# Performance work log

Hardware: AMD Instinct MI355X
Metric: run time of the kernel (lower is better)

Reference implementation:

```python
import jax, jax.numpy as jnp
import numpy as np

N_NODES = 50000   # number of graph nodes
N_EDGES = 800000  # avg degree 16
D_IN = 128
D_OUT = 128


def setup_inputs() -> dict:
    key = jax.random.key(0)
    k = jax.random.split(key, 5)
    seq = jax.random.normal(k[0], (N_NODES, D_IN), dtype=jnp.float32)
    # Linear weight, torch layout [out_dim, in_dim], xavier-ish scale
    W = jax.random.normal(k[1], (D_OUT, D_IN), dtype=jnp.float32) * (1.414 / np.sqrt(D_IN))
    b = jnp.zeros((D_OUT,), dtype=jnp.float32)  # bias init fill_(0.0)
    # COO sparse adjacency: out[row] += val * seq_proj[col]
    edge_row = jax.random.randint(k[2], (N_EDGES,), 0, N_NODES, dtype=jnp.int32)
    edge_col = jax.random.randint(k[3], (N_EDGES,), 0, N_NODES, dtype=jnp.int32)
    edge_val = jax.random.uniform(k[4], (N_EDGES,), dtype=jnp.float32)
    return {"seq": seq, "W": W, "b": b,
            "edge_row": edge_row, "edge_col": edge_col, "edge_val": edge_val}


def reference(seq, W, b, edge_row, edge_col, edge_val):
    # seq = self.fc(seq): [N, D_in] @ [D_in, D_out]
    h = seq @ W.T                                   # [N, D_out]
    # out = torch.spmm(adj, h): COO gather-scale-scatter
    msgs = h[edge_col] * edge_val[:, None]          # [E, D_out]
    out = jax.ops.segment_sum(msgs, edge_row, num_segments=N_NODES)  # [N, D_out]
    # bias add + relu (fused epilogue)
    return jax.nn.relu(out + b)
```

## Files before the change

### kernel.cpp

```cpp
#include <hip/hip_runtime.h>

#define NN 50000
#define NE 800000
#define DD 128

#define BK_SHIFT 8
#define NBUCK 196
#define CHUNK 2048
#define NCHUNK 391
#define NGB 782
#define ECAP 8192

#define OFF_H      0
#define OFF_EBIN   3200000
#define OFF_EPACK  6411264
#define OFF_END    9622528
#define OFF_CUR    9672528
#define WS_FULL_FLOATS 9672724

typedef short short8 __attribute__((ext_vector_type(8)));
typedef float f32x4 __attribute__((ext_vector_type(4)));
typedef unsigned int uint32x2 __attribute__((ext_vector_type(2)));

static __device__ __forceinline__ unsigned int f2bf(float x) {
    unsigned int u = __float_as_uint(x);
    return (u + 0x7fffu + ((u >> 16) & 1u)) >> 16;
}

__global__ __launch_bounds__(256) void k1_gemm_scatter(
        const float* __restrict__ seq, const float* __restrict__ W,
        unsigned short* __restrict__ h,
        const int* __restrict__ erow, const int* __restrict__ ecol,
        const float* __restrict__ eval,
        int* __restrict__ gcur, uint2* __restrict__ ebin) {
    __shared__ uint4 lds4[3072];
    char* lds = (char*)lds4;
    const int t = threadIdx.x;

    if (blockIdx.x < NCHUNK) {
        int* lh = (int*)lds4;
        const int chunk = blockIdx.x;
        for (int i = t; i < NBUCK; i += 256) lh[i] = 0;
        __syncthreads();
        const int e0 = chunk * CHUNK;
        for (int i = t; i < CHUNK; i += 256) {
            int e = e0 + i;
            if (e < NE) atomicAdd(&lh[erow[e] >> BK_SHIFT], 1);
        }
        __syncthreads();
        for (int i = t; i < NBUCK; i += 256) {
            int c = lh[i];
            lh[i] = c ? atomicAdd(&gcur[i], c) : 0;
        }
        __syncthreads();
        for (int i = t; i < CHUNK; i += 256) {
            int e = e0 + i;
            if (e < NE) {
                int r = erow[e], c = ecol[e];
                unsigned int vb = __float_as_uint(eval[e]);
                int k = r >> BK_SHIFT;
                int pos = atomicAdd(&lh[k], 1);
                if (pos < ECAP)
                    ebin[(size_t)k * ECAP + pos] =
                        make_uint2(((unsigned)r << 16) | (unsigned)c, vb);
            }
        }
        return;
    }

    const int base = (blockIdx.x - NCHUNK) * 64;
#define BS_OFF 16384

    {
        const int o = t >> 1, ksb = (t & 1) * 64;
        const float4* Wr = (const float4*)(W + o * 128 + ksb);
#pragma unroll
        for (int i = 0; i < 16; i += 2) {
            float4 x = Wr[i], y = Wr[i + 1];
            uint4 p;
            p.x = f2bf(x.x) | (f2bf(x.y) << 16);
            p.y = f2bf(x.z) | (f2bf(x.w) << 16);
            p.z = f2bf(y.x) | (f2bf(y.y) << 16);
            p.w = f2bf(y.z) | (f2bf(y.w) << 16);
            int byte = o * 256 + (ksb + i * 4) * 2;
            *(uint4*)(lds + BS_OFF + (byte ^ ((o & 7) << 4))) = p;
        }
    }
    {
        const int row = t >> 2, n = base + row;
        const int c0 = (t & 3) * 4;
        const float4* Sr = (const float4*)(seq + (size_t)n * 128);
        const bool ok = (n < NN);
#pragma unroll
        for (int i = 0; i < 4; ++i) {
            int cc = c0 + i;
            float4 x = ok ? Sr[cc * 2]     : make_float4(0.f, 0.f, 0.f, 0.f);
            float4 y = ok ? Sr[cc * 2 + 1] : make_float4(0.f, 0.f, 0.f, 0.f);
            uint4 p;
            p.x = f2bf(x.x) | (f2bf(x.y) << 16);
            p.y = f2bf(x.z) | (f2bf(x.w) << 16);
            p.z = f2bf(y.x) | (f2bf(y.y) << 16);
            p.w = f2bf(y.z) | (f2bf(y.w) << 16);
            int byte = row * 256 + cc * 16;
            *(uint4*)(lds + (byte ^ ((row & 7) << 4))) = p;
        }
    }
    __syncthreads();

    const int l = t & 63, wv = t >> 6;
    const int lr = l & 15, kg = l >> 4;
    const int arow = wv * 16 + lr;
    f32x4 acc[8] = {};

#pragma unroll
    for (int ks = 0; ks < 4; ++ks) {
        const int kbyte = ks * 64 + kg * 16;
        short8 av = *(short8*)(lds + ((arow * 256 + kbyte) ^ ((arow & 7) << 4)));
#pragma unroll
        for (int c = 0; c < 8; ++c) {
            const int o = c * 16 + lr;
            short8 bv = *(short8*)(lds + BS_OFF +
                                   ((o * 256 + kbyte) ^ ((o & 7) << 4)));
            acc[c] = __builtin_amdgcn_mfma_f32_16x16x32_bf16(av, bv, acc[c], 0, 0, 0);
        }
    }

#pragma unroll
    for (int c = 0; c < 8; ++c) {
#pragma unroll
        for (int r = 0; r < 4; ++r) {
            int n = base + wv * 16 + kg * 4 + r;
            if (n < NN)
                h[(size_t)n * DD + c * 16 + lr] = (unsigned short)f2bf(acc[c][r]);
        }
    }
}

__global__ __launch_bounds__(256) void csr_fill(const uint2* __restrict__ ebin,
                                                const int* __restrict__ gcur,
                                                int* __restrict__ endv,
                                                uint2* __restrict__ epack) {
    __shared__ int lh[256];
    __shared__ int lx[256];
    const int k = blockIdx.x;
    const int t = threadIdx.x;
    const size_t s0 = (size_t)k * ECAP;
    int cnt = gcur[k];
    if (cnt > ECAP) cnt = ECAP;
    const size_t s1 = s0 + cnt;
    const int r0 = k << BK_SHIFT;

    lh[t] = 0;
    __syncthreads();
    for (size_t e = s0 + t; e < s1; e += 256)
        atomicAdd(&lh[(ebin[e].x >> 16) & 255], 1);
    __syncthreads();

    const int myc = lh[t];
    lx[t] = myc;
    __syncthreads();
    for (int off = 1; off < 256; off <<= 1) {
        int y = (t >= off) ? lx[t - off] : 0;
        __syncthreads();
        lx[t] += y;
        __syncthreads();
    }
    const int incl = lx[t];
    const int row = r0 + t;
    if (row < NN) endv[row] = (int)s0 + incl;
    __syncthreads();
    lh[t] = (int)s0 + incl - myc;
    __syncthreads();

    for (size_t e = s0 + t; e < s1; e += 256) {
        uint2 ed = ebin[e];
        int pos = atomicAdd(&lh[(ed.x >> 16) & 255], 1);
        epack[pos] = make_uint2(ed.x & 0xffffu, ed.y);
    }
}

__global__ __launch_bounds__(256) void gather_kernel(const unsigned short* __restrict__ h,
                                                     const int* __restrict__ end,
                                                     const unsigned int* __restrict__ epack,
                                                     const float* __restrict__ b,
                                                     float* __restrict__ out) {
    const int row  = blockIdx.x * 4 + (threadIdx.x >> 6);
    const int lane = threadIdx.x & 63;
    const int slot = lane >> 4;
    const int sub  = lane & 15;
    const int begin = (row & 255) ? end[row - 1] : (row >> BK_SHIFT) * ECAP;
    const int e1 = end[row];

    float acc[8] = {0.f, 0.f, 0.f, 0.f, 0.f, 0.f, 0.f, 0.f};
    const unsigned short* hp = h + sub * 8;

#define BODY(EE) do {                                                          \
        uint32x2 cv = __builtin_nontemporal_load(                              \
            (const uint32x2*)(epack + (size_t)(EE) * 2));                      \
        float v = __uint_as_float(cv.y);                                       \
        uint4 hv = *(const uint4*)(hp + (size_t)cv.x * DD);                    \
        unsigned int uu;                                                       \
        uu = hv.x;                                                             \
        acc[0] = fmaf(v, __uint_as_float(uu << 16),          acc[0]);          \
        acc[1] = fmaf(v, __uint_as_float(uu & 0xffff0000u),  acc[1]);          \
        uu = hv.y;                                                             \
        acc[2] = fmaf(v, __uint_as_float(uu << 16),          acc[2]);          \
        acc[3] = fmaf(v, __uint_as_float(uu & 0xffff0000u),  acc[3]);          \
        uu = hv.z;                                                             \
        acc[4] = fmaf(v, __uint_as_float(uu << 16),          acc[4]);          \
        acc[5] = fmaf(v, __uint_as_float(uu & 0xffff0000u),  acc[5]);          \
        uu = hv.w;                                                             \
        acc[6] = fmaf(v, __uint_as_float(uu << 16),          acc[6]);          \
        acc[7] = fmaf(v, __uint_as_float(uu & 0xffff0000u),  acc[7]);          \
    } while (0)

    int e = begin + slot;
    for (; e + 12 < e1; e += 16) { BODY(e); BODY(e + 4); BODY(e + 8); BODY(e + 12); }
    for (; e < e1; e += 4) BODY(e);
#undef BODY

#pragma unroll
    for (int i = 0; i < 8; ++i) {
        acc[i] += __shfl_xor(acc[i], 16);
        acc[i] += __shfl_xor(acc[i], 32);
    }

    if (slot == 0) {
        const float4* b4 = (const float4*)(b + sub * 8);
        float4 b0 = b4[0], b1 = b4[1];
        f32x4 o0, o1;
        o0.x = fmaxf(acc[0] + b0.x, 0.f);
        o0.y = fmaxf(acc[1] + b0.y, 0.f);
        o0.z = fmaxf(acc[2] + b0.z, 0.f);
        o0.w = fmaxf(acc[3] + b0.w, 0.f);
        o1.x = fmaxf(acc[4] + b1.x, 0.f);
        o1.y = fmaxf(acc[5] + b1.y, 0.f);
        o1.z = fmaxf(acc[6] + b1.z, 0.f);
        o1.w = fmaxf(acc[7] + b1.w, 0.f);
        f32x4* op = (f32x4*)(out + (size_t)row * DD + sub * 8);
        __builtin_nontemporal_store(o0, op);
        __builtin_nontemporal_store(o1, op + 1);
    }
}

__global__ __launch_bounds__(256) void scatter_kernel(const unsigned short* __restrict__ h,
                                                      const int* __restrict__ erow,
                                                      const int* __restrict__ ecol,
                                                      const float* __restrict__ eval,
                                                      float* __restrict__ out) {
    const int lane   = threadIdx.x & 63;
    const int wave   = (blockIdx.x * blockDim.x + threadIdx.x) >> 6;
    const int nwaves = (gridDim.x * blockDim.x) >> 6;
    for (int e = wave; e < NE; e += nwaves) {
        int   r = erow[e];
        int   c = ecol[e];
        float v = eval[e];
        unsigned int u = *(const unsigned int*)&h[(size_t)c * DD + lane * 2];
        float* dst = &out[(size_t)r * DD + lane * 2];
        unsafeAtomicAdd(dst,     __uint_as_float(u << 16) * v);
        unsafeAtomicAdd(dst + 1, __uint_as_float(u & 0xffff0000u) * v);
    }
}

__global__ __launch_bounds__(256) void epilogue_kernel(float* __restrict__ out,
                                                       const float* __restrict__ b) {
    const float4* b4 = (const float4*)b;
    const int total4 = NN * DD / 4;
    int i = blockIdx.x * blockDim.x + threadIdx.x;
    for (; i < total4; i += gridDim.x * blockDim.x) {
        float4 x = ((float4*)out)[i];
        float4 bb = b4[i & 31];
        x.x = fmaxf(x.x + bb.x, 0.0f);
        x.y = fmaxf(x.y + bb.y, 0.0f);
        x.z = fmaxf(x.z + bb.z, 0.0f);
        x.w = fmaxf(x.w + bb.w, 0.0f);
        ((float4*)out)[i] = x;
    }
}

extern "C" void kernel_launch(void* const* d_in, const int* in_sizes, int n_in,
                              void* d_out, int out_size, void* d_ws, size_t ws_size,
                              hipStream_t stream) {
    const float* seq  = (const float*)d_in[0];
    const float* W    = (const float*)d_in[1];
    const float* b    = (const float*)d_in[2];
    const int*   erow = (const int*)d_in[3];
    const int*   ecol = (const int*)d_in[4];
    const float* eval = (const float*)d_in[5];
    float* out = (float*)d_out;

    float* wsf = (float*)d_ws;
    unsigned short* h = (unsigned short*)(wsf + OFF_H);
    uint2* ebin  = (uint2*)(wsf + OFF_EBIN);
    uint2* epack = (uint2*)(wsf + OFF_EPACK);
    int*   endv  = (int*)(wsf + OFF_END);
    int*   gcur  = (int*)(wsf + OFF_CUR);

    if (ws_size >= (size_t)WS_FULL_FLOATS * sizeof(float)) {
        hipMemsetAsync(gcur, 0, NBUCK * sizeof(int), stream);
        k1_gemm_scatter<<<NGB + NCHUNK, 256, 0, stream>>>(seq, W, h, erow, ecol,
                                                          eval, gcur, ebin);
        csr_fill<<<NBUCK, 256, 0, stream>>>(ebin, gcur, endv, epack);
        gather_kernel<<<NN / 4, 256, 0, stream>>>(h, endv, (const unsigned int*)epack, b, out);
    } else {
        k1_gemm_scatter<<<NGB + NCHUNK, 256, 0, stream>>>(seq, W, h, erow, ecol,
                                                          eval, gcur, ebin);
        hipMemsetAsync(out, 0, (size_t)out_size * sizeof(float), stream);
        scatter_kernel<<<4096, 256, 0, stream>>>(h, erow, ecol, eval, out);
        epilogue_kernel<<<2048, 256, 0, stream>>>(out, b);
    }
}
```

Measured before the change: 85.13 us.

## Move GEMM into CSR-fill kernel and pre-cast W to bf16 once

Restructures the stage schedule. The first kernel now only bins edges and casts W to bf16 once into workspace. The second kernel runs the per-bucket CSR fill and the dense GEMM blocks side by side, so the 196-block fill no longer runs alone and underfills the GPU. GEMM blocks now load the pre-cast bf16 W instead of each converting fp32 W themselves. The fallback path for small workspace is removed, so the code now assumes enough workspace is available.

Measured after the change: 84.70 us. About the same (-0.5%).

```diff
diff --git a/kernel.cpp b/kernel.cpp
--- a/kernel.cpp
+++ b/kernel.cpp
@@ -16,7 +16,8 @@
 #define OFF_EPACK  6411264
 #define OFF_END    9622528
 #define OFF_CUR    9672528
-#define WS_FULL_FLOATS 9672724
+#define OFF_WB     9672724
+#define WS_FULL_FLOATS 9680916
 
 typedef short short8 __attribute__((ext_vector_type(8)));
 typedef float f32x4 __attribute__((ext_vector_type(4)));
@@ -27,22 +28,18 @@
     return (u + 0x7fffu + ((u >> 16) & 1u)) >> 16;
 }
 
-__global__ __launch_bounds__(256) void k1_gemm_scatter(
-        const float* __restrict__ seq, const float* __restrict__ W,
-        unsigned short* __restrict__ h,
+__global__ __launch_bounds__(256) void k1_scatter_wcast(
+        const float* __restrict__ W, unsigned short* __restrict__ Wb,
         const int* __restrict__ erow, const int* __restrict__ ecol,
         const float* __restrict__ eval,
         int* __restrict__ gcur, uint2* __restrict__ ebin) {
-    __shared__ uint4 lds4[3072];
-    char* lds = (char*)lds4;
     const int t = threadIdx.x;
 
     if (blockIdx.x < NCHUNK) {
-        int* lh = (int*)lds4;
-        const int chunk = blockIdx.x;
+        __shared__ int lh[NBUCK];
         for (int i = t; i < NBUCK; i += 256) lh[i] = 0;
         __syncthreads();
-        const int e0 = chunk * CHUNK;
+        const int e0 = blockIdx.x * CHUNK;
         for (int i = t; i < CHUNK; i += 256) {
             int e = e0 + i;
             if (e < NE) atomicAdd(&lh[erow[e] >> BK_SHIFT], 1);
@@ -68,22 +65,77 @@
         return;
     }
 
-    const int base = (blockIdx.x - NCHUNK) * 64;
+    const float4* in4 = (const float4*)W;
+    uint4* out4 = (uint4*)Wb;
+    for (int i = t; i < 2048; i += 256) {
+        float4 x = in4[i * 2], y = in4[i * 2 + 1];
+        uint4 p;
+        p.x = f2bf(x.x) | (f2bf(x.y) << 16);
+        p.y = f2bf(x.z) | (f2bf(x.w) << 16);
+        p.z = f2bf(y.x) | (f2bf(y.y) << 16);
+        p.w = f2bf(y.z) | (f2bf(y.w) << 16);
+        out4[i] = p;
+    }
+}
+
+__global__ __launch_bounds__(256) void k2_fill_gemm(
+        const float* __restrict__ seq, const unsigned short* __restrict__ Wb,
+        unsigned short* __restrict__ h,
+        const uint2* __restrict__ ebin, const int* __restrict__ gcur,
+        int* __restrict__ endv, uint2* __restrict__ epack) {
+    __shared__ uint4 lds4[3072];
+    char* lds = (char*)lds4;
+    const int t = threadIdx.x;
+
+    if (blockIdx.x < NBUCK) {
+        int* lh = (int*)lds4;
+        int* lx = lh + 256;
+        const int k = blockIdx.x;
+        const size_t s0 = (size_t)k * ECAP;
+        int cnt = gcur[k];
+        if (cnt > ECAP) cnt = ECAP;
+        const size_t s1 = s0 + cnt;
+        const int r0 = k << BK_SHIFT;
+
+        lh[t] = 0;
+        __syncthreads();
+        for (size_t e = s0 + t; e < s1; e += 256)
+            atomicAdd(&lh[(ebin[e].x >> 16) & 255], 1);
+        __syncthreads();
+
+        const int myc = lh[t];
+        lx[t] = myc;
+        __syncthreads();
+        for (int off = 1; off < 256; off <<= 1) {
+            int y = (t >= off) ? lx[t - off] : 0;
+            __syncthreads();
+            lx[t] += y;
+            __syncthreads();
+        }
+        const int incl = lx[t];
+        const int row = r0 + t;
+        if (row < NN) endv[row] = (int)s0 + incl;
+        __syncthreads();
+        lh[t] = (int)s0 + incl - myc;
+        __syncthreads();
+
+        for (size_t e = s0 + t; e < s1; e += 256) {
+            uint2 ed = ebin[e];
+            int pos = atomicAdd(&lh[(ed.x >> 16) & 255], 1);
+            epack[pos] = make_uint2(ed.x & 0xffffu, ed.y);
+        }
+        return;
+    }
+
+    const int base = (blockIdx.x - NBUCK) * 64;
 #define BS_OFF 16384
 
     {
-        const int o = t >> 1, ksb = (t & 1) * 64;
-        const float4* Wr = (const float4*)(W + o * 128 + ksb);
-#pragma unroll
-        for (int i = 0; i < 16; i += 2) {
-            float4 x = Wr[i], y = Wr[i + 1];
-            uint4 p;
-            p.x = f2bf(x.x) | (f2bf(x.y) << 16);
-            p.y = f2bf(x.z) | (f2bf(x.w) << 16);
-            p.z = f2bf(y.x) | (f2bf(y.y) << 16);
-            p.w = f2bf(y.z) | (f2bf(y.w) << 16);
-            int byte = o * 256 + (ksb + i * 4) * 2;
-            *(uint4*)(lds + BS_OFF + (byte ^ ((o & 7) << 4))) = p;
+        const uint4* wg = (const uint4*)Wb;
+        for (int i = t; i < 2048; i += 256) {
+            int o = i >> 4, seg = i & 15;
+            int byte = o * 256 + seg * 16;
+            *(uint4*)(lds + BS_OFF + (byte ^ ((o & 7) << 4))) = wg[i];
         }
     }
     {
@@ -133,49 +185,6 @@
             if (n < NN)
                 h[(size_t)n * DD + c * 16 + lr] = (unsigned short)f2bf(acc[c][r]);
         }
-    }
-}
-
-__global__ __launch_bounds__(256) void csr_fill(const uint2* __restrict__ ebin,
-                                                const int* __restrict__ gcur,
-                                                int* __restrict__ endv,
-                                                uint2* __restrict__ epack) {
-    __shared__ int lh[256];
-    __shared__ int lx[256];
-    const int k = blockIdx.x;
-    const int t = threadIdx.x;
-    const size_t s0 = (size_t)k * ECAP;
-    int cnt = gcur[k];
-    if (cnt > ECAP) cnt = ECAP;
-    const size_t s1 = s0 + cnt;
-    const int r0 = k << BK_SHIFT;
-
-    lh[t] = 0;
-    __syncthreads();
-    for (size_t e = s0 + t; e < s1; e += 256)
-        atomicAdd(&lh[(ebin[e].x >> 16) & 255], 1);
-    __syncthreads();
-
-    const int myc = lh[t];
-    lx[t] = myc;
-    __syncthreads();
-    for (int off = 1; off < 256; off <<= 1) {
-        int y = (t >= off) ? lx[t - off] : 0;
-        __syncthreads();
-        lx[t] += y;
-        __syncthreads();
-    }
-    const int incl = lx[t];
-    const int row = r0 + t;
-    if (row < NN) endv[row] = (int)s0 + incl;
-    __syncthreads();
-    lh[t] = (int)s0 + incl - myc;
-    __syncthreads();
-
-    for (size_t e = s0 + t; e < s1; e += 256) {
-        uint2 ed = ebin[e];
-        int pos = atomicAdd(&lh[(ed.x >> 16) & 255], 1);
-        epack[pos] = make_uint2(ed.x & 0xffffu, ed.y);
     }
 }
 
@@ -243,41 +252,6 @@
     }
 }
 
-__global__ __launch_bounds__(256) void scatter_kernel(const unsigned short* __restrict__ h,
-                                                      const int* __restrict__ erow,
-                                                      const int* __restrict__ ecol,
-                                                      const float* __restrict__ eval,
-                                                      float* __restrict__ out) {
-    const int lane   = threadIdx.x & 63;
-    const int wave   = (blockIdx.x * blockDim.x + threadIdx.x) >> 6;
-    const int nwaves = (gridDim.x * blockDim.x) >> 6;
-    for (int e = wave; e < NE; e += nwaves) {
-        int   r = erow[e];
-        int   c = ecol[e];
-        float v = eval[e];
-        unsigned int u = *(const unsigned int*)&h[(size_t)c * DD + lane * 2];
-        float* dst = &out[(size_t)r * DD + lane * 2];
-        unsafeAtomicAdd(dst,     __uint_as_float(u << 16) * v);
-        unsafeAtomicAdd(dst + 1, __uint_as_float(u & 0xffff0000u) * v);
-    }
-}
-
-__global__ __launch_bounds__(256) void epilogue_kernel(float* __restrict__ out,
-                                                       const float* __restrict__ b) {
-    const float4* b4 = (const float4*)b;
-    const int total4 = NN * DD / 4;
-    int i = blockIdx.x * blockDim.x + threadIdx.x;
-    for (; i < total4; i += gridDim.x * blockDim.x) {
-        float4 x = ((float4*)out)[i];
-        float4 bb = b4[i & 31];
-        x.x = fmaxf(x.x + bb.x, 0.0f);
-        x.y = fmaxf(x.y + bb.y, 0.0f);
-        x.z = fmaxf(x.z + bb.z, 0.0f);
-        x.w = fmaxf(x.w + bb.w, 0.0f);
-        ((float4*)out)[i] = x;
-    }
-}
-
 extern "C" void kernel_launch(void* const* d_in, const int* in_sizes, int n_in,
                               void* d_out, int out_size, void* d_ws, size_t ws_size,
                               hipStream_t stream) {
@@ -290,23 +264,18 @@
     float* out = (float*)d_out;
 
     float* wsf = (float*)d_ws;
-    unsigned short* h = (unsigned short*)(wsf + OFF_H);
+    unsigned short* h  = (unsigned short*)(wsf + OFF_H);
     uint2* ebin  = (uint2*)(wsf + OFF_EBIN);
     uint2* epack = (uint2*)(wsf + OFF_EPACK);
     int*   endv  = (int*)(wsf + OFF_END);
     int*   gcur  = (int*)(wsf + OFF_CUR);
-
-    if (ws_size >= (size_t)WS_FULL_FLOATS * sizeof(float)) {
-        hipMemsetAsync(gcur, 0, NBUCK * sizeof(int), stream);
-        k1_gemm_scatter<<<NGB + NCHUNK, 256, 0, stream>>>(seq, W, h, erow, ecol,
-                                                          eval, gcur, ebin);
-        csr_fill<<<NBUCK, 256, 0, stream>>>(ebin, gcur, endv, epack);
-        gather_kernel<<<NN / 4, 256, 0, stream>>>(h, endv, (const unsigned int*)epack, b, out);
-    } else {
-        k1_gemm_scatter<<<NGB + NCHUNK, 256, 0, stream>>>(seq, W, h, erow, ecol,
-                                                          eval, gcur, ebin);
-        hipMemsetAsync(out, 0, (size_t)out_size * sizeof(float), stream);
-        scatter_kernel<<<4096, 256, 0, stream>>>(h, erow, ecol, eval, out);
-        epilogue_kernel<<<2048, 256, 0, stream>>>(out, b);
-    }
-}
+    unsigned short* Wb = (unsigned short*)(wsf + OFF_WB);
+
+    hipMemsetAsync(gcur, 0, NBUCK * sizeof(int), stream);
+    k1_scatter_wcast<<<NCHUNK + 1, 256, 0, stream>>>(W, Wb, erow, ecol, eval,
+                                                     gcur, ebin);
+    k2_fill_gemm<<<NBUCK + NGB, 256, 0, stream>>>(seq, Wb, h, ebin, gcur,
+                                                  endv, epack);
+    gather_kernel<<<NN / 4, 256, 0, stream>>>(h, endv, (const unsigned int*)epack,
+                                              b, out);
+}
```
